# Kernel optimization log

Hardware: AMD Instinct MI355X
Metric: run time of the kernel (lower is better)

## Reference

```python
import jax, jax.numpy as jnp
import numpy as np

B, N, K = 8, 1024, 1024
C1, C2 = 64, 128
EPS = 1e-5
XTOL = 1e-7


def _skew(w):
    x, y, z = w[..., 0], w[..., 1], w[..., 2]
    o = jnp.zeros_like(x)
    r0 = jnp.stack([o, -z, y], axis=-1)
    r1 = jnp.stack([z, o, -x], axis=-1)
    r2 = jnp.stack([-y, x, o], axis=-1)
    return jnp.stack([r0, r1, r2], axis=-2)


def _expmap(dx):
    # se(3) exponential map, twist = [w(3), v(3)] -> [B,4,4]
    w, v = dx[:, :3], dx[:, 3:]
    t = jnp.linalg.norm(w, axis=1)
    W = _skew(w)
    S = jnp.matmul(W, W)
    t2 = t * t
    small = t < 1e-4
    ts = jnp.where(small, jnp.ones_like(t), t)
    s1 = jnp.where(small, 1.0 - t2 / 6.0, jnp.sin(ts) / ts)            # sin(t)/t
    s2 = jnp.where(small, 0.5 - t2 / 24.0, (1.0 - jnp.cos(ts)) / (ts * ts))  # (1-cos t)/t^2
    s3 = jnp.where(small, 1.0 / 6.0 - t2 / 120.0, (ts - jnp.sin(ts)) / (ts * ts * ts))  # (t-sin t)/t^3
    I = jnp.eye(3, dtype=dx.dtype)
    R = I + s1[:, None, None] * W + s2[:, None, None] * S
    V = I + s2[:, None, None] * W + s3[:, None, None] * S
    p = jnp.einsum('bij,bj->bi', V, v)
    g = jnp.zeros((dx.shape[0], 4, 4), dtype=dx.dtype)
    g = g.at[:, :3, :3].set(R).at[:, :3, 3].set(p).at[:, 3, 3].set(1.0)
    return g


def _transform(g, p):
    # g: [B,4,4] rigid transforms, p: [B,N,3]
    return jnp.einsum('bij,bnj->bni', g[:, :3, :3], p) + g[:, None, :3, 3]


def _bn_eval(x, gamma, beta, rm, rv_):
    # eval-mode batchnorm over channel dim of [B,C,N]
    return gamma[:, None] * (x - rm[:, None]) * jax.lax.rsqrt(rv_[:, None] + EPS) + beta[:, None]


def _pointnet(p, params, with_jac=False):
    # shared-MLP PointNet: conv1x1 -> BN(eval) -> ReLU (x3), then max-pool over points
    x = jnp.swapaxes(p, 1, 2)  # [B,3,N]
    masks = []
    for (Wt, b, gamma, beta, rm, rv_) in params:
        x = jnp.einsum('oc,bcn->bon', Wt, x) + b[:, None]
        x = _bn_eval(x, gamma, beta, rm, rv_)
        x = jnp.maximum(x, 0.0)
        if with_jac:
            masks.append((x > 0.0).astype(x.dtype))
    f = jnp.max(x, axis=-1)  # [B,K]
    if with_jac:
        return f, masks, jnp.argmax(x, axis=-1)  # max_idx [B,K]
    return f


def _cal_pinv(p0, params, masks, max_idx):
    # analytical Jacobian (Cal_Jac) + Gauss-Newton pseudo-inverse
    bsz, npts = p0.shape[0], p0.shape[1]
    W1, W2, W3 = params[0][0], params[1][0], params[2][0]
    d1 = params[0][2] * jax.lax.rsqrt(params[0][5] + EPS)  # dBN/dx in eval mode (per channel)
    d2 = params[1][2] * jax.lax.rsqrt(params[1][5] + EPS)
    d3 = params[2][2] * jax.lax.rsqrt(params[2][5] + EPS)
    D1 = d1[None, :, None] * masks[0]  # [B,C1,N]
    D2 = d2[None, :, None] * masks[1]  # [B,C2,N]
    D3 = d3[None, :, None] * masks[2]  # [B,K,N]
    # feature jacobian chain d f / d p : [B,K,N,3]
    t1 = jnp.einsum('ci,bcn->bnic', W1, D1)            # [B,N,3,C1]
    t2 = jnp.einsum('bnic,dc,bdn->bnid', t1, W2, D2)   # [B,N,3,C2]
    fj = jnp.einsum('bnid,kd,bkn->bkni', t2, W3, D3)   # [B,K,N,3]
    # warp jacobian at identity twist: [-[p]x | -I3] -> [B,N,3,6]
    eye3 = jnp.broadcast_to(jnp.eye(3, dtype=p0.dtype), (bsz, npts, 3, 3))
    warp = jnp.concatenate([-_skew(p0), -eye3], axis=-1)
    # gather the argmax point per feature channel (only rows surviving max-pool)
    fjg = jnp.take_along_axis(fj, max_idx[:, :, None, None], axis=2)[:, :, 0, :]  # [B,K,3]
    wg = jnp.take_along_axis(warp.reshape(bsz, npts, 18), max_idx[:, :, None], axis=1)
    wg = wg.reshape(bsz, -1, 3, 6)  # [B,K,3,6]
    J = jnp.einsum('bki,bkim->bkm', fjg, wg)  # [B,K,6]
    H = jnp.einsum('bki,bkj->bij', J, J)      # [B,6,6]
    pinv = jnp.einsum('bij,bkj->bik', jnp.linalg.inv(H), J)  # [B,6,K]
    return pinv


def _forward(p0, p1, W1, b1, gamma1, beta1, rm1, rv1, W2, b2, gamma2, beta2, rm2, rv2, W3, b3, gamma3, beta3, rm3, rv3, maxiter):
    params = [(W1, b1, gamma1, beta1, rm1, rv1),
              (W2, b2, gamma2, beta2, rm2, rv2),
              (W3, b3, gamma3, beta3, rm3, rv3)]
    f0, masks, max_idx = _pointnet(p0, params, with_jac=True)
    pinv = _cal_pinv(p0, params, masks, max_idx)
    bsz = p0.shape[0]
    g0 = jnp.broadcast_to(jnp.eye(4, dtype=p0.dtype), (bsz, 4, 4))

    def step(carry, _):
        g, r, done = carry
        p = _transform(g, p1)
        f = _pointnet(p, params)
        r_new = jnp.where(done, r, f - f0)           # freeze residual after xtol break
        dx = jnp.einsum('bik,bk->bi', pinv, r_new)   # Gauss-Newton step [B,6]
        conv = jnp.max(jnp.linalg.norm(dx, axis=1)) < XTOL
        stop = done | conv
        g_new = jnp.where(stop, g, jnp.matmul(_expmap(dx), g))
        return (g_new, r_new, stop), None

    init = (g0, jnp.zeros_like(f0), jnp.array(False))
    (g, r, _), _ = jax.lax.scan(step, init, None, length=maxiter)
    return r


def setup_inputs():
    key = jax.random.key(0)
    ks = jax.random.split(key, 24)
    f32 = jnp.float32
    rn = lambda i, s, sc=1.0: jax.random.normal(ks[i], s, dtype=f32) * sc
    ru = lambda i, s: jax.random.uniform(ks[i], s, dtype=f32, minval=0.5, maxval=1.5)
    p0 = rn(0, (B, N, 3))
    inp = {
        'p0': p0,
        'p1': p0 + rn(1, (B, N, 3), 0.02),  # small rigid-ish perturbation -> meaningful registration
        'W1': rn(2, (C1, 3), 0.5), 'b1': rn(3, (C1,), 0.1),
        'gamma1': ru(4, (C1,)), 'beta1': rn(5, (C1,), 0.1),
        'rm1': rn(6, (C1,), 0.1), 'rv1': ru(7, (C1,)),
        'W2': rn(8, (C2, C1), 0.2), 'b2': rn(9, (C2,), 0.1),
        'gamma2': ru(10, (C2,)), 'beta2': rn(11, (C2,), 0.1),
        'rm2': rn(12, (C2,), 0.1), 'rv2': ru(13, (C2,)),
        'W3': rn(14, (K, C2), 0.1), 'b3': rn(15, (K,), 0.1),
        'gamma3': ru(16, (K,)), 'beta3': rn(17, (K,), 0.1),
        'rm3': rn(18, (K,), 0.1), 'rv3': ru(19, (K,)),
        'maxiter': 10,
    }
    return inp


def reference(p0, p1, W1, b1, gamma1, beta1, rm1, rv1, W2, b2, gamma2, beta2, rm2, rv2, W3, b3, gamma3, beta3, rm3, rv3, maxiter):
    return _forward(p0, p1, W1, b1, gamma1, beta1, rm1, rv1, W2, b2, gamma2, beta2, rm2, rv2, W3, b3, gamma3, beta3, rm3, rv3, maxiter)
```

## Files before the change

kernel.cpp:

```cpp
#include <hip/hip_runtime.h>

#define B_ 8
#define N_ 1024
#define C1_ 64
#define C2_ 128
#define K_ 1024
#define EPS_ 1e-5f
#define XTOL_ 1e-7f

#define OFF_G      0
#define OFF_F0     128
#define OFF_PM     8320
#define OFF_M1     24704
#define OFF_M2     41088
#define OFF_SC3    73856
#define OFF_OFF3   74880
#define OFF_OFF2   75904
#define OFF_W1F    76032
#define OFF_W3HI   76288
#define OFF_W3LO   141824
#define OFF_W2H    207360
#define OFF_W2L    211456
#define OFF_J      215552
#define OFF_PINVT  264704
#define OFF_PART   330240
#define OFF_DXG    461312
#define OFF_NRM    461360
#define OFF_CNT    461368

typedef __attribute__((ext_vector_type(8))) short bf16x8;
typedef __attribute__((ext_vector_type(4))) float f32x4;

static __device__ inline unsigned short f2bf(float x) {
    unsigned u = __float_as_uint(x);
    unsigned r = (u + 0x7FFFu + ((u >> 16) & 1u)) >> 16;
    return (unsigned short)r;
}
static __device__ inline float bf2f(unsigned short h) {
    return __uint_as_float(((unsigned)h) << 16);
}
static __device__ inline unsigned pk2(unsigned short a, unsigned short b) {
    return (unsigned)a | ((unsigned)b << 16);
}

__global__ __launch_bounds__(256)
void k_prep(const float* __restrict__ W3, const float* __restrict__ b3,
            const float* __restrict__ ga3, const float* __restrict__ be3,
            const float* __restrict__ rm3, const float* __restrict__ rv3,
            const float* __restrict__ W1, const float* __restrict__ b1,
            const float* __restrict__ ga1, const float* __restrict__ be1,
            const float* __restrict__ rm1, const float* __restrict__ rv1,
            const float* __restrict__ W2, const float* __restrict__ b2,
            const float* __restrict__ ga2, const float* __restrict__ be2,
            const float* __restrict__ rm2, const float* __restrict__ rv2,
            unsigned short* __restrict__ w3hi, unsigned short* __restrict__ w3lo,
            float* __restrict__ sc3, float* __restrict__ off3,
            unsigned short* __restrict__ w2h, unsigned short* __restrict__ w2l,
            float* __restrict__ off2, float* __restrict__ w1f,
            unsigned int* __restrict__ cnt) {
    int gid = blockIdx.x * 256 + threadIdx.x;
    if (gid < K_ * C2_) {
        float w = W3[gid];
        unsigned short h = f2bf(w);
        w3hi[gid] = h;
        w3lo[gid] = f2bf(w - bf2f(h));
    }
    if (gid < K_) {
        float sc = ga3[gid] * rsqrtf(rv3[gid] + EPS_);
        sc3[gid] = sc;
        off3[gid] = sc * (b3[gid] - rm3[gid]) + be3[gid];
    }
    if (gid < C2_ * C1_) {
        int o = gid >> 6, c = gid & 63;
        float sc = ga2[o] * rsqrtf(rv2[o] + EPS_);
        float v = W2[o * C1_ + c] * sc;
        unsigned short h = f2bf(v);
        w2h[o * C1_ + c] = h;
        w2l[o * C1_ + c] = f2bf(v - bf2f(h));
    }
    if (gid < C2_) {
        float sc = ga2[gid] * rsqrtf(rv2[gid] + EPS_);
        off2[gid] = sc * (b2[gid] - rm2[gid]) + be2[gid];
    }
    if (gid < C1_) {
        float sc = ga1[gid] * rsqrtf(rv1[gid] + EPS_);
        w1f[gid * 4 + 0] = W1[gid * 3 + 0] * sc;
        w1f[gid * 4 + 1] = W1[gid * 3 + 1] * sc;
        w1f[gid * 4 + 2] = W1[gid * 3 + 2] * sc;
        w1f[gid * 4 + 3] = sc * (b1[gid] - rm1[gid]) + be1[gid];
    }
    if (gid == 0) *cnt = 0u;
}

template<int MODE>
__global__ __launch_bounds__(1024, 4)
void k_fused(const float* __restrict__ pts, const float* __restrict__ g,
             const float* __restrict__ w1f,
             const unsigned short* __restrict__ w2h, const unsigned short* __restrict__ w2l,
             const float* __restrict__ off2,
             const unsigned short* __restrict__ w3hi, const unsigned short* __restrict__ w3lo,
             const float* __restrict__ sc3, const float* __restrict__ off3,
             unsigned long long* __restrict__ part,
             unsigned long long* __restrict__ m1b, unsigned int* __restrict__ m2q) {
    __shared__ __align__(16) unsigned short a1h[128][72];
    __shared__ __align__(16) unsigned short a1l[128][72];
    __shared__ __align__(16) unsigned short sB[2][128][136];
    __shared__ float sSc[256], sOff[256], sOff2[C2_];
    __shared__ unsigned int m1w[2][128];
    __shared__ unsigned int m2w[4][128];
    __shared__ unsigned long long pmL[256];

    int slab = blockIdx.x;
    int b    = blockIdx.y;
    int q    = blockIdx.z;
    int n0   = slab * 128;
    int tx   = threadIdx.x;
    int w    = tx >> 6;
    int l    = tx & 63;
    int l15  = l & 15;
    int lhi  = l >> 4;

    if (tx < 256) { sSc[tx] = sc3[q * 256 + tx]; sOff[tx] = off3[q * 256 + tx]; }
    if (tx < C2_) sOff2[tx] = off2[tx];
    if (MODE == 0 && tx < 128) {
        m1w[0][tx] = 0u; m1w[1][tx] = 0u;
        m2w[0][tx] = 0u; m2w[1][tx] = 0u; m2w[2][tx] = 0u; m2w[3][tx] = 0u;
    }
    __syncthreads();

    {
        int n = tx & 127;
        int cgi = tx >> 7;
        const float* pp = pts + (b * N_ + n0 + n) * 3;
        float px = pp[0], py = pp[1], pz = pp[2];
        float q0, q1, q2;
        if (MODE == 1) {
            const float* gb = g + b * 16;
            q0 = fmaf(gb[0], px, fmaf(gb[1], py, fmaf(gb[2],  pz, gb[3])));
            q1 = fmaf(gb[4], px, fmaf(gb[5], py, fmaf(gb[6],  pz, gb[7])));
            q2 = fmaf(gb[8], px, fmaf(gb[9], py, fmaf(gb[10], pz, gb[11])));
        } else {
            q0 = px; q1 = py; q2 = pz;
        }
        unsigned int bits = 0u;
        unsigned hw[4], lw[4];
        #pragma unroll
        for (int j = 0; j < 8; ++j) {
            int c = cgi * 8 + j;
            float4 wf = *(const float4*)(w1f + c * 4);
            float y = fmaxf(fmaf(wf.x, q0, fmaf(wf.y, q1, fmaf(wf.z, q2, wf.w))), 0.f);
            unsigned short h = f2bf(y);
            unsigned short lo = f2bf(y - bf2f(h));
            if (j & 1) { hw[j >> 1] |= ((unsigned)h) << 16; lw[j >> 1] |= ((unsigned)lo) << 16; }
            else       { hw[j >> 1] = (unsigned)h;          lw[j >> 1] = (unsigned)lo; }
            if (MODE == 0) bits |= ((unsigned int)(y > 0.f)) << j;
        }
        uint4 vh; vh.x = hw[0]; vh.y = hw[1]; vh.z = hw[2]; vh.w = hw[3];
        uint4 vl; vl.x = lw[0]; vl.y = lw[1]; vl.z = lw[2]; vl.w = lw[3];
        *(uint4*)&a1h[n][cgi * 8] = vh;
        *(uint4*)&a1l[n][cgi * 8] = vl;
        if (MODE == 0) atomicOr(&m1w[cgi >> 2][n], bits << ((cgi & 3) * 8));
    }
    __syncthreads();

    {
        int og = w & 7;
        int nh = (w >> 3) * 4;
        f32x4 acc2[4];
        #pragma unroll
        for (int nfi = 0; nfi < 4; ++nfi) acc2[nfi] = (f32x4){0.f, 0.f, 0.f, 0.f};
        #pragma unroll
        for (int ks = 0; ks < 2; ++ks) {
            int k0 = ks * 32;
            int aoff = (og * 16 + l15) * C1_ + k0 + lhi * 8;
            bf16x8 ah2 = *(const bf16x8*)(w2h + aoff);
            bf16x8 al2 = *(const bf16x8*)(w2l + aoff);
            #pragma unroll
            for (int nfi = 0; nfi < 4; ++nfi) {
                int n = (nh + nfi) * 16 + l15;
                bf16x8 bh2 = *(const bf16x8*)&a1h[n][k0 + lhi * 8];
                bf16x8 bl2 = *(const bf16x8*)&a1l[n][k0 + lhi * 8];
                acc2[nfi] = __builtin_amdgcn_mfma_f32_16x16x32_bf16(ah2, bh2, acc2[nfi], 0, 0, 0);
                acc2[nfi] = __builtin_amdgcn_mfma_f32_16x16x32_bf16(ah2, bl2, acc2[nfi], 0, 0, 0);
                acc2[nfi] = __builtin_amdgcn_mfma_f32_16x16x32_bf16(al2, bh2, acc2[nfi], 0, 0, 0);
            }
        }
        #pragma unroll
        for (int nfi = 0; nfi < 4; ++nfi) {
            int n = (nh + nfi) * 16 + l15;
            unsigned short h4[4], l4[4];
            #pragma unroll
            for (int r = 0; r < 4; ++r) {
                int o = og * 16 + lhi * 4 + r;
                float y = fmaxf(acc2[nfi][r] + sOff2[o], 0.f);
                unsigned short h = f2bf(y);
                h4[r] = h;
                l4[r] = f2bf(y - bf2f(h));
                if (MODE == 0 && y > 0.f) atomicOr(&m2w[o >> 5][n], 1u << (o & 31));
            }
            uint2 vh; vh.x = pk2(h4[0], h4[1]); vh.y = pk2(h4[2], h4[3]);
            uint2 vl; vl.x = pk2(l4[0], l4[1]); vl.y = pk2(l4[2], l4[3]);
            *(uint2*)&sB[0][n][og * 16 + lhi * 4] = vh;
            *(uint2*)&sB[1][n][og * 16 + lhi * 4] = vl;
        }
    }
    __syncthreads();

    if (MODE == 0 && q == 0 && tx < 128) {
        m1b[b * N_ + n0 + tx] =
            (unsigned long long)m1w[0][tx] | ((unsigned long long)m1w[1][tx] << 32);
        uint4 mv; mv.x = m2w[0][tx]; mv.y = m2w[1][tx]; mv.z = m2w[2][tx]; mv.w = m2w[3][tx];
        *(uint4*)&m2q[(b * N_ + n0 + tx) * 4] = mv;
    }

    f32x4 acc[8];
    #pragma unroll
    for (int nf = 0; nf < 8; ++nf) acc[nf] = (f32x4){0.f, 0.f, 0.f, 0.f};

    #pragma unroll
    for (int ks = 0; ks < 4; ++ks) {
        int k0 = ks * 32;
        int orow = q * 256 + w * 16 + l15;
        int off = orow * C2_ + k0 + lhi * 8;
        bf16x8 ah = *(const bf16x8*)(w3hi + off);
        bf16x8 al = *(const bf16x8*)(w3lo + off);
        #pragma unroll
        for (int nh = 0; nh < 2; ++nh) {
            bf16x8 bh[4], bl[4];
            #pragma unroll
            for (int nfi = 0; nfi < 4; ++nfi) {
                int n = (nh * 4 + nfi) * 16 + l15;
                bh[nfi] = *(const bf16x8*)&sB[0][n][k0 + lhi * 8];
                bl[nfi] = *(const bf16x8*)&sB[1][n][k0 + lhi * 8];
            }
            #pragma unroll
            for (int nfi = 0; nfi < 4; ++nfi) {
                int nf = nh * 4 + nfi;
                acc[nf] = __builtin_amdgcn_mfma_f32_16x16x32_bf16(ah, bh[nfi], acc[nf], 0, 0, 0);
                acc[nf] = __builtin_amdgcn_mfma_f32_16x16x32_bf16(ah, bl[nfi], acc[nf], 0, 0, 0);
                acc[nf] = __builtin_amdgcn_mfma_f32_16x16x32_bf16(al, bh[nfi], acc[nf], 0, 0, 0);
            }
        }
    }

    #pragma unroll
    for (int r = 0; r < 4; ++r) {
        int o_l = w * 16 + lhi * 4 + r;
        float sc = sSc[o_l], of = sOff[o_l];
        float bv = -3.4e38f;
        int bi = 0;
        #pragma unroll
        for (int nf = 0; nf < 8; ++nf) {
            float y = fmaxf(sc * acc[nf][r] + of, 0.f);
            int nn = n0 + nf * 16 + l15;
            if (y > bv) { bv = y; bi = nn; }
        }
        #pragma unroll
        for (int m = 1; m <= 8; m <<= 1) {
            float ov = __shfl_xor(bv, m);
            int oi = __shfl_xor(bi, m);
            if (ov > bv || (ov == bv && oi < bi)) { bv = ov; bi = oi; }
        }
        if (l15 == 0) {
            pmL[o_l] = ((unsigned long long)__float_as_uint(bv) << 32)
                     | (unsigned int)(~(unsigned int)bi);
        }
    }
    __syncthreads();
    if (tx < 256)
        part[(size_t)slab * (B_ * K_) + b * K_ + q * 256 + tx] = pmL[tx];
}

__global__ __launch_bounds__(256)
void k_reduce(const unsigned long long* __restrict__ part,
              unsigned long long* __restrict__ pm) {
    int gid = blockIdx.x * 256 + threadIdx.x;
    unsigned long long m = part[gid];
    #pragma unroll
    for (int s = 1; s < 8; ++s) {
        unsigned long long v = part[(size_t)s * (B_ * K_) + gid];
        m = (v > m) ? v : m;
    }
    pm[gid] = m;
}

__global__ __launch_bounds__(256)
void k_rdx(const unsigned long long* __restrict__ part,
           const float* __restrict__ f0, const float* __restrict__ pinvT,
           float* __restrict__ out, float* __restrict__ g,
           float* __restrict__ dxg, float* __restrict__ nrmg,
           unsigned int* __restrict__ cnt) {
    __shared__ float redB[4][6];
    __shared__ int isLast;
    int bb = blockIdx.x;
    int tx = threadIdx.x;
    int w = tx >> 6;
    int l = tx & 63;

    float acc[6] = {0.f, 0.f, 0.f, 0.f, 0.f, 0.f};
    #pragma unroll
    for (int half = 0; half < 4; ++half) {
        int o = half * 256 + tx;
        unsigned long long m = part[(size_t)bb * K_ + o];
        #pragma unroll
        for (int s = 1; s < 8; ++s) {
            unsigned long long v = part[(size_t)s * (B_ * K_) + bb * K_ + o];
            m = (v > m) ? v : m;
        }
        float fv = __uint_as_float((unsigned int)(m >> 32));
        float rv = fv - f0[bb * K_ + o];
        out[bb * K_ + o] = rv;
        const float4* pp = (const float4*)(pinvT + (size_t)(bb * K_ + o) * 8);
        float4 pa = pp[0], pb = pp[1];
        acc[0] += pa.x * rv; acc[1] += pa.y * rv; acc[2] += pa.z * rv;
        acc[3] += pa.w * rv; acc[4] += pb.x * rv; acc[5] += pb.y * rv;
    }
    #pragma unroll
    for (int i = 0; i < 6; ++i)
        for (int off = 32; off > 0; off >>= 1) acc[i] += __shfl_down(acc[i], off);
    if (l == 0) {
        #pragma unroll
        for (int i = 0; i < 6; ++i) redB[w][i] = acc[i];
    }
    __syncthreads();
    if (tx == 0) {
        float dx6[6];
        #pragma unroll
        for (int i = 0; i < 6; ++i) {
            dx6[i] = redB[0][i] + redB[1][i] + redB[2][i] + redB[3][i];
            atomicExch(&dxg[bb * 6 + i], dx6[i]);
        }
        atomicExch(&nrmg[bb],
                   sqrtf(dx6[0]*dx6[0] + dx6[1]*dx6[1] + dx6[2]*dx6[2]
                       + dx6[3]*dx6[3] + dx6[4]*dx6[4] + dx6[5]*dx6[5]));
    }
    __threadfence();
    __syncthreads();
    if (tx == 0) {
        unsigned int old = atomicAdd(cnt, 1u);
        isLast = (old == B_ - 1) ? 1 : 0;
        if (isLast) atomicExch(cnt, 0u);
    }
    __syncthreads();
    if (!isLast) return;

    if (tx < B_) {
        int b = tx;
        float mx = 0.f;
        #pragma unroll
        for (int i = 0; i < B_; ++i) mx = fmaxf(mx, atomicAdd(&nrmg[i], 0.f));
        if (mx < XTOL_) return;
        float d[6];
        #pragma unroll
        for (int i = 0; i < 6; ++i) d[i] = atomicAdd(&dxg[b * 6 + i], 0.f);
        float wx = d[0], wy = d[1], wz = d[2];
        float vx = d[3], vy = d[4], vz = d[5];
        float t2 = wx*wx + wy*wy + wz*wz;
        float t = sqrtf(t2);
        float s1, s2, s3;
        if (t < 1e-4f) {
            s1 = 1.f - t2 / 6.f;
            s2 = 0.5f - t2 / 24.f;
            s3 = 1.f / 6.f - t2 / 120.f;
        } else {
            float st = sinf(t), ct = cosf(t);
            s1 = st / t;
            s2 = (1.f - ct) / t2;
            s3 = (t - st) / (t2 * t);
        }
        float W[3][3] = {{0.f, -wz, wy}, {wz, 0.f, -wx}, {-wy, wx, 0.f}};
        float S[3][3];
        #pragma unroll
        for (int i = 0; i < 3; ++i)
            #pragma unroll
            for (int j = 0; j < 3; ++j)
                S[i][j] = W[i][0]*W[0][j] + W[i][1]*W[1][j] + W[i][2]*W[2][j];
        float R[3][3], V[3][3];
        #pragma unroll
        for (int i = 0; i < 3; ++i)
            #pragma unroll
            for (int j = 0; j < 3; ++j) {
                float id = (i == j) ? 1.f : 0.f;
                R[i][j] = id + s1 * W[i][j] + s2 * S[i][j];
                V[i][j] = id + s2 * W[i][j] + s3 * S[i][j];
            }
        float p[3];
        #pragma unroll
        for (int i = 0; i < 3; ++i) p[i] = V[i][0]*vx + V[i][1]*vy + V[i][2]*vz;
        float* gb = g + b * 16;
        float go[16];
        #pragma unroll
        for (int i = 0; i < 16; ++i) go[i] = gb[i];
        #pragma unroll
        for (int i = 0; i < 3; ++i)
            #pragma unroll
            for (int j = 0; j < 4; ++j)
                gb[i * 4 + j] = R[i][0]*go[0*4+j] + R[i][1]*go[1*4+j]
                              + R[i][2]*go[2*4+j] + p[i]*go[3*4+j];
    }
}

__global__ __launch_bounds__(256)
void k_jac(const float* __restrict__ p0,
           const unsigned long long* __restrict__ m1b,
           const unsigned int* __restrict__ m2q,
           const float* __restrict__ W1, const float* __restrict__ ga1, const float* __restrict__ rv1,
           const float* __restrict__ W2, const float* __restrict__ ga2, const float* __restrict__ rv2,
           const float* __restrict__ W3, const float* __restrict__ ga3, const float* __restrict__ rv3,
           const unsigned long long* __restrict__ pm,
           float* __restrict__ f0, float* __restrict__ J) {
    __shared__ float wvs[4][128];
    int tx = threadIdx.x;
    int wv = tx >> 6;
    int l = tx & 63;
    int w = blockIdx.x * 4 + wv;
    int b = w >> 10;
    int k = w & 1023;

    unsigned long long pk = pm[b * K_ + k];
    float f0v = __uint_as_float((unsigned int)(pk >> 32));
    int ns = (int)(~(unsigned int)pk);
    if (l == 0) f0[b * K_ + k] = f0v;

    unsigned long long m1 = m1b[b * N_ + ns];
    const unsigned int* mq = m2q + (b * N_ + ns) * 4;
    unsigned int qa = mq[0], qb = mq[1], qc = mq[2], qd = mq[3];
    unsigned int blo = (l < 32) ? (qa >> l) : (qb >> (l - 32));
    unsigned int bhi = (l < 32) ? (qc >> l) : (qd >> (l - 32));

    const float* w3r = W3 + k * C2_;
    float s2a = ga2[l] * rsqrtf(rv2[l] + EPS_);
    float s2b = ga2[64 + l] * rsqrtf(rv2[64 + l] + EPS_);
    float wa = (blo & 1u) ? w3r[l] * s2a : 0.f;
    float wb = (bhi & 1u) ? w3r[64 + l] * s2b : 0.f;
    wvs[wv][l] = wa;
    wvs[wv][64 + l] = wb;
    __syncthreads();

    float v = 0.f;
    #pragma unroll 8
    for (int d = 0; d < C2_; ++d) v += wvs[wv][d] * W2[d * C1_ + l];

    float d1l = ((m1 >> l) & 1ull) ? ga1[l] * rsqrtf(rv1[l] + EPS_) : 0.f;
    float vc = v * d1l;
    float fj0 = vc * W1[l * 3 + 0];
    float fj1 = vc * W1[l * 3 + 1];
    float fj2 = vc * W1[l * 3 + 2];
    #pragma unroll
    for (int off = 32; off; off >>= 1) {
        fj0 += __shfl_xor(fj0, off);
        fj1 += __shfl_xor(fj1, off);
        fj2 += __shfl_xor(fj2, off);
    }
    if (l == 0) {
        float D3 = (f0v > 0.f) ? ga3[k] * rsqrtf(rv3[k] + EPS_) : 0.f;
        fj0 *= D3; fj1 *= D3; fj2 *= D3;
        float x = p0[(b * N_ + ns) * 3 + 0];
        float y = p0[(b * N_ + ns) * 3 + 1];
        float z = p0[(b * N_ + ns) * 3 + 2];
        float* Jr = J + (b * K_ + k) * 6;
        Jr[0] = fj1 * (-z) + fj2 * y;
        Jr[1] = fj0 * z    + fj2 * (-x);
        Jr[2] = fj0 * (-y) + fj1 * x;
        Jr[3] = -fj0;
        Jr[4] = -fj1;
        Jr[5] = -fj2;
    }
}

__global__ void k_hpinv(const float* __restrict__ J, float* __restrict__ pinvT,
                        float* __restrict__ g) {
    int b = blockIdx.x;
    int tx = threadIdx.x;
    __shared__ float red[256][22];
    __shared__ float hinv[36];

    if (tx < 16) g[b * 16 + tx] = (tx % 5 == 0) ? 1.f : 0.f;

    float h[21];
    #pragma unroll
    for (int q = 0; q < 21; ++q) h[q] = 0.f;
    for (int k = tx; k < K_; k += 256) {
        const float* Jr = J + (b * K_ + k) * 6;
        float jv[6] = {Jr[0], Jr[1], Jr[2], Jr[3], Jr[4], Jr[5]};
        int q = 0;
        #pragma unroll
        for (int i = 0; i < 6; ++i)
            #pragma unroll
            for (int jj = i; jj < 6; ++jj) h[q++] += jv[i] * jv[jj];
    }
    #pragma unroll
    for (int q = 0; q < 21; ++q) red[tx][q] = h[q];
    __syncthreads();
    for (int s = 128; s > 0; s >>= 1) {
        if (tx < s)
            for (int q = 0; q < 21; ++q) red[tx][q] += red[tx + s][q];
        __syncthreads();
    }
    if (tx == 0) {
        float A[6][6], Inv[6][6];
        {
            int q = 0;
            #pragma unroll
            for (int i = 0; i < 6; ++i)
                #pragma unroll
                for (int jj = i; jj < 6; ++jj) { A[i][jj] = red[0][q]; A[jj][i] = red[0][q]; ++q; }
        }
        #pragma unroll
        for (int i = 0; i < 6; ++i)
            #pragma unroll
            for (int jj = 0; jj < 6; ++jj) Inv[i][jj] = (i == jj) ? 1.f : 0.f;
        #pragma unroll
        for (int col = 0; col < 6; ++col) {
            float ipv = 1.f / A[col][col];
            #pragma unroll
            for (int jj = 0; jj < 6; ++jj) { A[col][jj] *= ipv; Inv[col][jj] *= ipv; }
            #pragma unroll
            for (int r2 = 0; r2 < 6; ++r2) {
                if (r2 == col) continue;
                float f = A[r2][col];
                #pragma unroll
                for (int jj = 0; jj < 6; ++jj) {
                    A[r2][jj]   -= f * A[col][jj];
                    Inv[r2][jj] -= f * Inv[col][jj];
                }
            }
        }
        #pragma unroll
        for (int i = 0; i < 6; ++i)
            #pragma unroll
            for (int jj = 0; jj < 6; ++jj) hinv[i * 6 + jj] = Inv[i][jj];
    }
    __syncthreads();
    for (int k = tx; k < K_; k += 256) {
        const float* Jr = J + (b * K_ + k) * 6;
        float j0 = Jr[0], j1 = Jr[1], j2 = Jr[2], j3 = Jr[3], j4 = Jr[4], j5 = Jr[5];
        float* pr = pinvT + (b * K_ + k) * 8;
        #pragma unroll
        for (int i = 0; i < 6; ++i) {
            pr[i] = hinv[i * 6 + 0] * j0 + hinv[i * 6 + 1] * j1 + hinv[i * 6 + 2] * j2
                  + hinv[i * 6 + 3] * j3 + hinv[i * 6 + 4] * j4 + hinv[i * 6 + 5] * j5;
        }
        pr[6] = 0.f; pr[7] = 0.f;
    }
}

extern "C" void kernel_launch(void* const* d_in, const int* in_sizes, int n_in,
                              void* d_out, int out_size, void* d_ws, size_t ws_size,
                              hipStream_t stream) {
    const float* p0  = (const float*)d_in[0];
    const float* p1  = (const float*)d_in[1];
    const float* W1  = (const float*)d_in[2];
    const float* b1  = (const float*)d_in[3];
    const float* ga1 = (const float*)d_in[4];
    const float* be1 = (const float*)d_in[5];
    const float* rm1 = (const float*)d_in[6];
    const float* rv1 = (const float*)d_in[7];
    const float* W2  = (const float*)d_in[8];
    const float* b2  = (const float*)d_in[9];
    const float* ga2 = (const float*)d_in[10];
    const float* be2 = (const float*)d_in[11];
    const float* rm2 = (const float*)d_in[12];
    const float* rv2 = (const float*)d_in[13];
    const float* W3  = (const float*)d_in[14];
    const float* b3  = (const float*)d_in[15];
    const float* ga3 = (const float*)d_in[16];
    const float* be3 = (const float*)d_in[17];
    const float* rm3 = (const float*)d_in[18];
    const float* rv3 = (const float*)d_in[19];

    float* ws   = (float*)d_ws;
    float* g    = ws + OFF_G;
    float* f0   = ws + OFF_F0;
    unsigned long long* pm  = (unsigned long long*)(ws + OFF_PM);
    unsigned long long* m1b = (unsigned long long*)(ws + OFF_M1);
    unsigned int*       m2q = (unsigned int*)(ws + OFF_M2);
    float* sc3  = ws + OFF_SC3;
    float* off3 = ws + OFF_OFF3;
    float* off2 = ws + OFF_OFF2;
    float* w1f  = ws + OFF_W1F;
    unsigned short* w3hi = (unsigned short*)(ws + OFF_W3HI);
    unsigned short* w3lo = (unsigned short*)(ws + OFF_W3LO);
    unsigned short* w2h  = (unsigned short*)(ws + OFF_W2H);
    unsigned short* w2l  = (unsigned short*)(ws + OFF_W2L);
    float* Jb    = ws + OFF_J;
    float* pinvT = ws + OFF_PINVT;
    unsigned long long* part = (unsigned long long*)(ws + OFF_PART);
    float* dxg   = ws + OFF_DXG;
    float* nrmg  = ws + OFF_NRM;
    unsigned int* cnt = (unsigned int*)(ws + OFF_CNT);
    float* out   = (float*)d_out;

    dim3 gridF(8, B_, 4);

    k_prep<<<(K_ * C2_ + 255) / 256, 256, 0, stream>>>(
        W3, b3, ga3, be3, rm3, rv3,
        W1, b1, ga1, be1, rm1, rv1,
        W2, b2, ga2, be2, rm2, rv2,
        w3hi, w3lo, sc3, off3, w2h, w2l, off2, w1f, cnt);

    k_fused<0><<<gridF, 1024, 0, stream>>>(p0, g, w1f, w2h, w2l, off2, w3hi, w3lo,
                                           sc3, off3, part, m1b, m2q);
    k_reduce<<<B_ * K_ / 256, 256, 0, stream>>>(part, pm);
    k_jac<<<B_ * K_ / 4, 256, 0, stream>>>(p0, m1b, m2q, W1, ga1, rv1, W2, ga2, rv2,
                                           W3, ga3, rv3, pm, f0, Jb);
    k_hpinv<<<B_, 256, 0, stream>>>(Jb, pinvT, g);

    for (int it = 0; it < 10; ++it) {
        k_fused<1><<<gridF, 1024, 0, stream>>>(p1, g, w1f, w2h, w2l, off2, w3hi, w3lo,
                                               sc3, off3, part, m1b, m2q);
        k_rdx<<<B_, 256, 0, stream>>>(part, f0, pinvT, out, g, dxg, nrmg, cnt);
    }
}
```

Baseline: 257.7 us.

## Split fused MLP into two point halves to cut LDS and registers

The fused layer-2/layer-3 stage now handles the 128-point slab in two halves of 64 points. This halves the shared sB buffer and replaces the 8-wide accumulator array with a single running accumulator plus running max/argmax. The launch bound rises from 4 to 8 waves per EU, which pushes the compiler toward fewer registers per thread. The cost is reloading W2/W3 fragments per half and per tile, plus extra barriers and less ILP inside each wave.

```diff
diff --git a/kernel.cpp b/kernel.cpp
--- a/kernel.cpp
+++ b/kernel.cpp
@@ -93,7 +93,7 @@
 }
 
 template<int MODE>
-__global__ __launch_bounds__(1024, 4)
+__global__ __launch_bounds__(1024, 8)
 void k_fused(const float* __restrict__ pts, const float* __restrict__ g,
              const float* __restrict__ w1f,
              const unsigned short* __restrict__ w2h, const unsigned short* __restrict__ w2l,
@@ -104,7 +104,7 @@
              unsigned long long* __restrict__ m1b, unsigned int* __restrict__ m2q) {
     __shared__ __align__(16) unsigned short a1h[128][72];
     __shared__ __align__(16) unsigned short a1l[128][72];
-    __shared__ __align__(16) unsigned short sB[2][128][136];
+    __shared__ __align__(16) unsigned short sB[2][64][136];
     __shared__ float sSc[256], sOff[256], sOff2[C2_];
     __shared__ unsigned int m1w[2][128];
     __shared__ unsigned int m2w[4][128];
@@ -163,107 +163,110 @@
     }
     __syncthreads();
 
-    {
-        int og = w & 7;
-        int nh = (w >> 3) * 4;
-        f32x4 acc2[4];
-        #pragma unroll
-        for (int nfi = 0; nfi < 4; ++nfi) acc2[nfi] = (f32x4){0.f, 0.f, 0.f, 0.f};
-        #pragma unroll
-        for (int ks = 0; ks < 2; ++ks) {
-            int k0 = ks * 32;
-            int aoff = (og * 16 + l15) * C1_ + k0 + lhi * 8;
-            bf16x8 ah2 = *(const bf16x8*)(w2h + aoff);
-            bf16x8 al2 = *(const bf16x8*)(w2l + aoff);
-            #pragma unroll
-            for (int nfi = 0; nfi < 4; ++nfi) {
-                int n = (nh + nfi) * 16 + l15;
-                bf16x8 bh2 = *(const bf16x8*)&a1h[n][k0 + lhi * 8];
-                bf16x8 bl2 = *(const bf16x8*)&a1l[n][k0 + lhi * 8];
-                acc2[nfi] = __builtin_amdgcn_mfma_f32_16x16x32_bf16(ah2, bh2, acc2[nfi], 0, 0, 0);
-                acc2[nfi] = __builtin_amdgcn_mfma_f32_16x16x32_bf16(ah2, bl2, acc2[nfi], 0, 0, 0);
-                acc2[nfi] = __builtin_amdgcn_mfma_f32_16x16x32_bf16(al2, bh2, acc2[nfi], 0, 0, 0);
-            }
-        }
-        #pragma unroll
-        for (int nfi = 0; nfi < 4; ++nfi) {
-            int n = (nh + nfi) * 16 + l15;
-            unsigned short h4[4], l4[4];
-            #pragma unroll
-            for (int r = 0; r < 4; ++r) {
-                int o = og * 16 + lhi * 4 + r;
-                float y = fmaxf(acc2[nfi][r] + sOff2[o], 0.f);
-                unsigned short h = f2bf(y);
-                h4[r] = h;
-                l4[r] = f2bf(y - bf2f(h));
-                if (MODE == 0 && y > 0.f) atomicOr(&m2w[o >> 5][n], 1u << (o & 31));
-            }
-            uint2 vh; vh.x = pk2(h4[0], h4[1]); vh.y = pk2(h4[2], h4[3]);
-            uint2 vl; vl.x = pk2(l4[0], l4[1]); vl.y = pk2(l4[2], l4[3]);
-            *(uint2*)&sB[0][n][og * 16 + lhi * 4] = vh;
-            *(uint2*)&sB[1][n][og * 16 + lhi * 4] = vl;
-        }
-    }
-    __syncthreads();
-
     if (MODE == 0 && q == 0 && tx < 128) {
         m1b[b * N_ + n0 + tx] =
             (unsigned long long)m1w[0][tx] | ((unsigned long long)m1w[1][tx] << 32);
+    }
+
+    float bv0 = -3.4e38f, bv1 = -3.4e38f, bv2 = -3.4e38f, bv3 = -3.4e38f;
+    int   bi0 = 0, bi1 = 0, bi2 = 0, bi3 = 0;
+    float scr[4], ofr[4];
+    #pragma unroll
+    for (int r = 0; r < 4; ++r) {
+        scr[r] = sSc[w * 16 + lhi * 4 + r];
+        ofr[r] = sOff[w * 16 + lhi * 4 + r];
+    }
+
+    for (int half = 0; half < 2; ++half) {
+        {
+            int og = w & 7;
+            #pragma unroll
+            for (int ti = 0; ti < 2; ++ti) {
+                int nf_l = (w >> 3) * 2 + ti;
+                int n_l = nf_l * 16 + l15;
+                int n_g = half * 64 + n_l;
+                f32x4 acc2 = (f32x4){0.f, 0.f, 0.f, 0.f};
+                #pragma unroll
+                for (int ks = 0; ks < 2; ++ks) {
+                    int k0 = ks * 32;
+                    int aoff = (og * 16 + l15) * C1_ + k0 + lhi * 8;
+                    bf16x8 ah2 = *(const bf16x8*)(w2h + aoff);
+                    bf16x8 al2 = *(const bf16x8*)(w2l + aoff);
+                    bf16x8 bh2 = *(const bf16x8*)&a1h[n_g][k0 + lhi * 8];
+                    bf16x8 bl2 = *(const bf16x8*)&a1l[n_g][k0 + lhi * 8];
+                    acc2 = __builtin_amdgcn_mfma_f32_16x16x32_bf16(ah2, bh2, acc2, 0, 0, 0);
+                    acc2 = __builtin_amdgcn_mfma_f32_16x16x32_bf16(ah2, bl2, acc2, 0, 0, 0);
+                    acc2 = __builtin_amdgcn_mfma_f32_16x16x32_bf16(al2, bh2, acc2, 0, 0, 0);
+                }
+                unsigned short h4[4], l4[4];
+                #pragma unroll
+                for (int r = 0; r < 4; ++r) {
+                    int o = og * 16 + lhi * 4 + r;
+                    float y = fmaxf(acc2[r] + sOff2[o], 0.f);
+                    unsigned short h = f2bf(y);
+                    h4[r] = h;
+                    l4[r] = f2bf(y - bf2f(h));
+                    if (MODE == 0 && y > 0.f) atomicOr(&m2w[o >> 5][n_g], 1u << (o & 31));
+                }
+                uint2 vh; vh.x = pk2(h4[0], h4[1]); vh.y = pk2(h4[2], h4[3]);
+                uint2 vl; vl.x = pk2(l4[0], l4[1]); vl.y = pk2(l4[2], l4[3]);
+                *(uint2*)&sB[0][n_l][og * 16 + lhi * 4] = vh;
+                *(uint2*)&sB[1][n_l][og * 16 + lhi * 4] = vl;
+            }
+        }
+        __syncthreads();
+
+        #pragma unroll
+        for (int nf_l = 0; nf_l < 4; ++nf_l) {
+            int n_l = nf_l * 16 + l15;
+            f32x4 acc = (f32x4){0.f, 0.f, 0.f, 0.f};
+            #pragma unroll
+            for (int ks = 0; ks < 4; ++ks) {
+                int k0 = ks * 32;
+                int orow = q * 256 + w * 16 + l15;
+                int off = orow * C2_ + k0 + lhi * 8;
+                bf16x8 ah = *(const bf16x8*)(w3hi + off);
+                bf16x8 al = *(const bf16x8*)(w3lo + off);
+                bf16x8 bh = *(const bf16x8*)&sB[0][n_l][k0 + lhi * 8];
+                bf16x8 bl = *(const bf16x8*)&sB[1][n_l][k0 + lhi * 8];
+                acc = __builtin_amdgcn_mfma_f32_16x16x32_bf16(ah, bh, acc, 0, 0, 0);
+                acc = __builtin_amdgcn_mfma_f32_16x16x32_bf16(ah, bl, acc, 0, 0, 0);
+                acc = __builtin_amdgcn_mfma_f32_16x16x32_bf16(al, bh, acc, 0, 0, 0);
+            }
+            int nn = n0 + half * 64 + nf_l * 16 + l15;
+            float y0 = fmaxf(scr[0] * acc[0] + ofr[0], 0.f);
+            float y1 = fmaxf(scr[1] * acc[1] + ofr[1], 0.f);
+            float y2 = fmaxf(scr[2] * acc[2] + ofr[2], 0.f);
+            float y3 = fmaxf(scr[3] * acc[3] + ofr[3], 0.f);
+            if (y0 > bv0) { bv0 = y0; bi0 = nn; }
+            if (y1 > bv1) { bv1 = y1; bi1 = nn; }
+            if (y2 > bv2) { bv2 = y2; bi2 = nn; }
+            if (y3 > bv3) { bv3 = y3; bi3 = nn; }
+        }
+        __syncthreads();
+    }
+
+    if (MODE == 0 && q == 0 && tx < 128) {
         uint4 mv; mv.x = m2w[0][tx]; mv.y = m2w[1][tx]; mv.z = m2w[2][tx]; mv.w = m2w[3][tx];
         *(uint4*)&m2q[(b * N_ + n0 + tx) * 4] = mv;
     }
 
-    f32x4 acc[8];
-    #pragma unroll
-    for (int nf = 0; nf < 8; ++nf) acc[nf] = (f32x4){0.f, 0.f, 0.f, 0.f};
-
-    #pragma unroll
-    for (int ks = 0; ks < 4; ++ks) {
-        int k0 = ks * 32;
-        int orow = q * 256 + w * 16 + l15;
-        int off = orow * C2_ + k0 + lhi * 8;
-        bf16x8 ah = *(const bf16x8*)(w3hi + off);
-        bf16x8 al = *(const bf16x8*)(w3lo + off);
-        #pragma unroll
-        for (int nh = 0; nh < 2; ++nh) {
-            bf16x8 bh[4], bl[4];
-            #pragma unroll
-            for (int nfi = 0; nfi < 4; ++nfi) {
-                int n = (nh * 4 + nfi) * 16 + l15;
-                bh[nfi] = *(const bf16x8*)&sB[0][n][k0 + lhi * 8];
-                bl[nfi] = *(const bf16x8*)&sB[1][n][k0 + lhi * 8];
+    {
+        float bv[4] = {bv0, bv1, bv2, bv3};
+        int   bi[4] = {bi0, bi1, bi2, bi3};
+        #pragma unroll
+        for (int r = 0; r < 4; ++r) {
+            #pragma unroll
+            for (int m = 1; m <= 8; m <<= 1) {
+                float ov = __shfl_xor(bv[r], m);
+                int oi = __shfl_xor(bi[r], m);
+                if (ov > bv[r] || (ov == bv[r] && oi < bi[r])) { bv[r] = ov; bi[r] = oi; }
             }
-            #pragma unroll
-            for (int nfi = 0; nfi < 4; ++nfi) {
-                int nf = nh * 4 + nfi;
-                acc[nf] = __builtin_amdgcn_mfma_f32_16x16x32_bf16(ah, bh[nfi], acc[nf], 0, 0, 0);
-                acc[nf] = __builtin_amdgcn_mfma_f32_16x16x32_bf16(ah, bl[nfi], acc[nf], 0, 0, 0);
-                acc[nf] = __builtin_amdgcn_mfma_f32_16x16x32_bf16(al, bh[nfi], acc[nf], 0, 0, 0);
+            if (l15 == 0) {
+                pmL[w * 16 + lhi * 4 + r] =
+                    ((unsigned long long)__float_as_uint(bv[r]) << 32)
+                    | (unsigned int)(~(unsigned int)bi[r]);
             }
-        }
-    }
-
-    #pragma unroll
-    for (int r = 0; r < 4; ++r) {
-        int o_l = w * 16 + lhi * 4 + r;
-        float sc = sSc[o_l], of = sOff[o_l];
-        float bv = -3.4e38f;
-        int bi = 0;
-        #pragma unroll
-        for (int nf = 0; nf < 8; ++nf) {
-            float y = fmaxf(sc * acc[nf][r] + of, 0.f);
-            int nn = n0 + nf * 16 + l15;
-            if (y > bv) { bv = y; bi = nn; }
-        }
-        #pragma unroll
-        for (int m = 1; m <= 8; m <<= 1) {
-            float ov = __shfl_xor(bv, m);
-            int oi = __shfl_xor(bi, m);
-            if (ov > bv || (ov == bv && oi < bi)) { bv = ov; bi = oi; }
-        }
-        if (l15 == 0) {
-            pmL[o_l] = ((unsigned long long)__float_as_uint(bv) << 32)
-                     | (unsigned int)(~(unsigned int)bi);
         }
     }
     __syncthreads();
```

Result: slower. 407.9 us (+58.3%).

## Retile fused PointNet kernel to 256-point slabs and 128-channel output groups

Applied to the files above, without the earlier changes.

Changes the fused kernel's work split from 8 point-slabs × 4 output quarters to 4 point-slabs of 256 × 8 output groups of 128. Each block now processes its slab in two halves, recomputing layer 2 per half and keeping running argmax in registers. This halves the number of partial-max slabs the reduce kernels must combine and gives more reuse of each slab's layer-1 activations. In exchange, layer 2 is recomputed across 8 output groups instead of 4, which doubles the redundant conv2 work, and the larger layer-1 shared buffers raise LDS use.

```diff
diff --git a/kernel.cpp b/kernel.cpp
--- a/kernel.cpp
+++ b/kernel.cpp
@@ -102,35 +102,36 @@
              const float* __restrict__ sc3, const float* __restrict__ off3,
              unsigned long long* __restrict__ part,
              unsigned long long* __restrict__ m1b, unsigned int* __restrict__ m2q) {
-    __shared__ __align__(16) unsigned short a1h[128][72];
-    __shared__ __align__(16) unsigned short a1l[128][72];
+    __shared__ __align__(16) unsigned short a1h[256][72];
+    __shared__ __align__(16) unsigned short a1l[256][72];
     __shared__ __align__(16) unsigned short sB[2][128][136];
-    __shared__ float sSc[256], sOff[256], sOff2[C2_];
-    __shared__ unsigned int m1w[2][128];
-    __shared__ unsigned int m2w[4][128];
-    __shared__ unsigned long long pmL[256];
+    __shared__ float sSc[128], sOff[128], sOff2[C2_];
+    __shared__ unsigned int m1w[2][256];
+    __shared__ unsigned int m2w[4][256];
+    __shared__ unsigned long long pmW[2][128];
 
     int slab = blockIdx.x;
     int b    = blockIdx.y;
-    int q    = blockIdx.z;
-    int n0   = slab * 128;
+    int oq   = blockIdx.z;
+    int n0   = slab * 256;
+    int ob   = oq * 128;
     int tx   = threadIdx.x;
     int w    = tx >> 6;
     int l    = tx & 63;
     int l15  = l & 15;
     int lhi  = l >> 4;
 
-    if (tx < 256) { sSc[tx] = sc3[q * 256 + tx]; sOff[tx] = off3[q * 256 + tx]; }
+    if (tx < 128) { sSc[tx] = sc3[ob + tx]; sOff[tx] = off3[ob + tx]; }
     if (tx < C2_) sOff2[tx] = off2[tx];
-    if (MODE == 0 && tx < 128) {
+    if (MODE == 0 && tx < 256) {
         m1w[0][tx] = 0u; m1w[1][tx] = 0u;
         m2w[0][tx] = 0u; m2w[1][tx] = 0u; m2w[2][tx] = 0u; m2w[3][tx] = 0u;
     }
     __syncthreads();
 
     {
-        int n = tx & 127;
-        int cgi = tx >> 7;
+        int n = tx & 255;
+        int cgi = tx >> 8;
         const float* pp = pts + (b * N_ + n0 + n) * 3;
         float px = pp[0], py = pp[1], pz = pp[2];
         float q0, q1, q2;
@@ -143,10 +144,10 @@
             q0 = px; q1 = py; q2 = pz;
         }
         unsigned int bits = 0u;
-        unsigned hw[4], lw[4];
-        #pragma unroll
-        for (int j = 0; j < 8; ++j) {
-            int c = cgi * 8 + j;
+        unsigned hw[8], lw[8];
+        #pragma unroll
+        for (int j = 0; j < 16; ++j) {
+            int c = cgi * 16 + j;
             float4 wf = *(const float4*)(w1f + c * 4);
             float y = fmaxf(fmaf(wf.x, q0, fmaf(wf.y, q1, fmaf(wf.z, q2, wf.w))), 0.f);
             unsigned short h = f2bf(y);
@@ -155,106 +156,120 @@
             else       { hw[j >> 1] = (unsigned)h;          lw[j >> 1] = (unsigned)lo; }
             if (MODE == 0) bits |= ((unsigned int)(y > 0.f)) << j;
         }
-        uint4 vh; vh.x = hw[0]; vh.y = hw[1]; vh.z = hw[2]; vh.w = hw[3];
-        uint4 vl; vl.x = lw[0]; vl.y = lw[1]; vl.z = lw[2]; vl.w = lw[3];
-        *(uint4*)&a1h[n][cgi * 8] = vh;
-        *(uint4*)&a1l[n][cgi * 8] = vl;
-        if (MODE == 0) atomicOr(&m1w[cgi >> 2][n], bits << ((cgi & 3) * 8));
-    }
-    __syncthreads();
-
-    {
-        int og = w & 7;
-        int nh = (w >> 3) * 4;
-        f32x4 acc2[4];
-        #pragma unroll
-        for (int nfi = 0; nfi < 4; ++nfi) acc2[nfi] = (f32x4){0.f, 0.f, 0.f, 0.f};
-        #pragma unroll
-        for (int ks = 0; ks < 2; ++ks) {
-            int k0 = ks * 32;
-            int aoff = (og * 16 + l15) * C1_ + k0 + lhi * 8;
-            bf16x8 ah2 = *(const bf16x8*)(w2h + aoff);
-            bf16x8 al2 = *(const bf16x8*)(w2l + aoff);
+        uint4 v0; v0.x = hw[0]; v0.y = hw[1]; v0.z = hw[2]; v0.w = hw[3];
+        uint4 v1; v1.x = hw[4]; v1.y = hw[5]; v1.z = hw[6]; v1.w = hw[7];
+        *(uint4*)&a1h[n][cgi * 16 + 0] = v0;
+        *(uint4*)&a1h[n][cgi * 16 + 8] = v1;
+        uint4 v2; v2.x = lw[0]; v2.y = lw[1]; v2.z = lw[2]; v2.w = lw[3];
+        uint4 v3; v3.x = lw[4]; v3.y = lw[5]; v3.z = lw[6]; v3.w = lw[7];
+        *(uint4*)&a1l[n][cgi * 16 + 0] = v2;
+        *(uint4*)&a1l[n][cgi * 16 + 8] = v3;
+        if (MODE == 0) atomicOr(&m1w[cgi >> 1][n], bits << ((cgi & 1) * 16));
+    }
+    __syncthreads();
+
+    int og3 = w & 7;
+    int nfh = w >> 3;
+    float bvr[4];
+    int   bir[4];
+    float scr[4], ofr[4];
+    #pragma unroll
+    for (int r = 0; r < 4; ++r) {
+        bvr[r] = -3.4e38f; bir[r] = 0;
+        scr[r] = sSc[og3 * 16 + lhi * 4 + r];
+        ofr[r] = sOff[og3 * 16 + lhi * 4 + r];
+    }
+
+    for (int half = 0; half < 2; ++half) {
+        {
+            int og = w & 7;
+            int nh = (w >> 3) * 4;
+            f32x4 acc2[4];
+            #pragma unroll
+            for (int nfi = 0; nfi < 4; ++nfi) acc2[nfi] = (f32x4){0.f, 0.f, 0.f, 0.f};
+            #pragma unroll
+            for (int ks = 0; ks < 2; ++ks) {
+                int k0 = ks * 32;
+                int aoff = (og * 16 + l15) * C1_ + k0 + lhi * 8;
+                bf16x8 ah2 = *(const bf16x8*)(w2h + aoff);
+                bf16x8 al2 = *(const bf16x8*)(w2l + aoff);
+                #pragma unroll
+                for (int nfi = 0; nfi < 4; ++nfi) {
+                    int n_g = half * 128 + (nh + nfi) * 16 + l15;
+                    bf16x8 bh2 = *(const bf16x8*)&a1h[n_g][k0 + lhi * 8];
+                    bf16x8 bl2 = *(const bf16x8*)&a1l[n_g][k0 + lhi * 8];
+                    acc2[nfi] = __builtin_amdgcn_mfma_f32_16x16x32_bf16(ah2, bh2, acc2[nfi], 0, 0, 0);
+                    acc2[nfi] = __builtin_amdgcn_mfma_f32_16x16x32_bf16(ah2, bl2, acc2[nfi], 0, 0, 0);
+                    acc2[nfi] = __builtin_amdgcn_mfma_f32_16x16x32_bf16(al2, bh2, acc2[nfi], 0, 0, 0);
+                }
+            }
             #pragma unroll
             for (int nfi = 0; nfi < 4; ++nfi) {
-                int n = (nh + nfi) * 16 + l15;
-                bf16x8 bh2 = *(const bf16x8*)&a1h[n][k0 + lhi * 8];
-                bf16x8 bl2 = *(const bf16x8*)&a1l[n][k0 + lhi * 8];
-                acc2[nfi] = __builtin_amdgcn_mfma_f32_16x16x32_bf16(ah2, bh2, acc2[nfi], 0, 0, 0);
-                acc2[nfi] = __builtin_amdgcn_mfma_f32_16x16x32_bf16(ah2, bl2, acc2[nfi], 0, 0, 0);
-                acc2[nfi] = __builtin_amdgcn_mfma_f32_16x16x32_bf16(al2, bh2, acc2[nfi], 0, 0, 0);
+                int n_l = (nh + nfi) * 16 + l15;
+                int n_g = half * 128 + n_l;
+                unsigned short h4[4], l4[4];
+                #pragma unroll
+                for (int r = 0; r < 4; ++r) {
+                    int o = og * 16 + lhi * 4 + r;
+                    float y = fmaxf(acc2[nfi][r] + sOff2[o], 0.f);
+                    unsigned short h = f2bf(y);
+                    h4[r] = h;
+                    l4[r] = f2bf(y - bf2f(h));
+                    if (MODE == 0 && y > 0.f) atomicOr(&m2w[o >> 5][n_g], 1u << (o & 31));
+                }
+                uint2 vh; vh.x = pk2(h4[0], h4[1]); vh.y = pk2(h4[2], h4[3]);
+                uint2 vl; vl.x = pk2(l4[0], l4[1]); vl.y = pk2(l4[2], l4[3]);
+                *(uint2*)&sB[0][n_l][og * 16 + lhi * 4] = vh;
+                *(uint2*)&sB[1][n_l][og * 16 + lhi * 4] = vl;
             }
         }
-        #pragma unroll
-        for (int nfi = 0; nfi < 4; ++nfi) {
-            int n = (nh + nfi) * 16 + l15;
-            unsigned short h4[4], l4[4];
-            #pragma unroll
-            for (int r = 0; r < 4; ++r) {
-                int o = og * 16 + lhi * 4 + r;
-                float y = fmaxf(acc2[nfi][r] + sOff2[o], 0.f);
-                unsigned short h = f2bf(y);
-                h4[r] = h;
-                l4[r] = f2bf(y - bf2f(h));
-                if (MODE == 0 && y > 0.f) atomicOr(&m2w[o >> 5][n], 1u << (o & 31));
+        __syncthreads();
+
+        {
+            f32x4 acc3[4];
+            #pragma unroll
+            for (int nfi = 0; nfi < 4; ++nfi) acc3[nfi] = (f32x4){0.f, 0.f, 0.f, 0.f};
+            #pragma unroll
+            for (int ks = 0; ks < 4; ++ks) {
+                int k0 = ks * 32;
+                int orow = ob + og3 * 16 + l15;
+                int off = orow * C2_ + k0 + lhi * 8;
+                bf16x8 ah = *(const bf16x8*)(w3hi + off);
+                bf16x8 al = *(const bf16x8*)(w3lo + off);
+                #pragma unroll
+                for (int nfi = 0; nfi < 4; ++nfi) {
+                    int n_l = (nfh * 4 + nfi) * 16 + l15;
+                    bf16x8 bh = *(const bf16x8*)&sB[0][n_l][k0 + lhi * 8];
+                    bf16x8 bl = *(const bf16x8*)&sB[1][n_l][k0 + lhi * 8];
+                    acc3[nfi] = __builtin_amdgcn_mfma_f32_16x16x32_bf16(ah, bh, acc3[nfi], 0, 0, 0);
+                    acc3[nfi] = __builtin_amdgcn_mfma_f32_16x16x32_bf16(ah, bl, acc3[nfi], 0, 0, 0);
+                    acc3[nfi] = __builtin_amdgcn_mfma_f32_16x16x32_bf16(al, bh, acc3[nfi], 0, 0, 0);
+                }
             }
-            uint2 vh; vh.x = pk2(h4[0], h4[1]); vh.y = pk2(h4[2], h4[3]);
-            uint2 vl; vl.x = pk2(l4[0], l4[1]); vl.y = pk2(l4[2], l4[3]);
-            *(uint2*)&sB[0][n][og * 16 + lhi * 4] = vh;
-            *(uint2*)&sB[1][n][og * 16 + lhi * 4] = vl;
-        }
-    }
-    __syncthreads();
-
-    if (MODE == 0 && q == 0 && tx < 128) {
+            #pragma unroll
+            for (int nfi = 0; nfi < 4; ++nfi) {
+                int nn = n0 + half * 128 + (nfh * 4 + nfi) * 16 + l15;
+                #pragma unroll
+                for (int r = 0; r < 4; ++r) {
+                    float y = fmaxf(scr[r] * acc3[nfi][r] + ofr[r], 0.f);
+                    if (y > bvr[r]) { bvr[r] = y; bir[r] = nn; }
+                }
+            }
+        }
+        __syncthreads();
+    }
+
+    if (MODE == 0 && oq == 0 && tx < 256) {
         m1b[b * N_ + n0 + tx] =
             (unsigned long long)m1w[0][tx] | ((unsigned long long)m1w[1][tx] << 32);
         uint4 mv; mv.x = m2w[0][tx]; mv.y = m2w[1][tx]; mv.z = m2w[2][tx]; mv.w = m2w[3][tx];
         *(uint4*)&m2q[(b * N_ + n0 + tx) * 4] = mv;
     }
 
-    f32x4 acc[8];
-    #pragma unroll
-    for (int nf = 0; nf < 8; ++nf) acc[nf] = (f32x4){0.f, 0.f, 0.f, 0.f};
-
-    #pragma unroll
-    for (int ks = 0; ks < 4; ++ks) {
-        int k0 = ks * 32;
-        int orow = q * 256 + w * 16 + l15;
-        int off = orow * C2_ + k0 + lhi * 8;
-        bf16x8 ah = *(const bf16x8*)(w3hi + off);
-        bf16x8 al = *(const bf16x8*)(w3lo + off);
-        #pragma unroll
-        for (int nh = 0; nh < 2; ++nh) {
-            bf16x8 bh[4], bl[4];
-            #pragma unroll
-            for (int nfi = 0; nfi < 4; ++nfi) {
-                int n = (nh * 4 + nfi) * 16 + l15;
-                bh[nfi] = *(const bf16x8*)&sB[0][n][k0 + lhi * 8];
-                bl[nfi] = *(const bf16x8*)&sB[1][n][k0 + lhi * 8];
-            }
-            #pragma unroll
-            for (int nfi = 0; nfi < 4; ++nfi) {
-                int nf = nh * 4 + nfi;
-                acc[nf] = __builtin_amdgcn_mfma_f32_16x16x32_bf16(ah, bh[nfi], acc[nf], 0, 0, 0);
-                acc[nf] = __builtin_amdgcn_mfma_f32_16x16x32_bf16(ah, bl[nfi], acc[nf], 0, 0, 0);
-                acc[nf] = __builtin_amdgcn_mfma_f32_16x16x32_bf16(al, bh[nfi], acc[nf], 0, 0, 0);
-            }
-        }
-    }
-
     #pragma unroll
     for (int r = 0; r < 4; ++r) {
-        int o_l = w * 16 + lhi * 4 + r;
-        float sc = sSc[o_l], of = sOff[o_l];
-        float bv = -3.4e38f;
-        int bi = 0;
-        #pragma unroll
-        for (int nf = 0; nf < 8; ++nf) {
-            float y = fmaxf(sc * acc[nf][r] + of, 0.f);
-            int nn = n0 + nf * 16 + l15;
-            if (y > bv) { bv = y; bi = nn; }
-        }
+        float bv = bvr[r];
+        int bi = bir[r];
         #pragma unroll
         for (int m = 1; m <= 8; m <<= 1) {
             float ov = __shfl_xor(bv, m);
@@ -262,13 +277,17 @@
             if (ov > bv || (ov == bv && oi < bi)) { bv = ov; bi = oi; }
         }
         if (l15 == 0) {
-            pmL[o_l] = ((unsigned long long)__float_as_uint(bv) << 32)
-                     | (unsigned int)(~(unsigned int)bi);
-        }
-    }
-    __syncthreads();
-    if (tx < 256)
-        part[(size_t)slab * (B_ * K_) + b * K_ + q * 256 + tx] = pmL[tx];
+            pmW[nfh][og3 * 16 + lhi * 4 + r] =
+                ((unsigned long long)__float_as_uint(bv) << 32)
+                | (unsigned int)(~(unsigned int)bi);
+        }
+    }
+    __syncthreads();
+    if (tx < 128) {
+        unsigned long long a = pmW[0][tx], c = pmW[1][tx];
+        unsigned long long m = (c > a) ? c : a;
+        part[(size_t)slab * (B_ * K_) + b * K_ + ob + tx] = m;
+    }
 }
 
 __global__ __launch_bounds__(256)
@@ -277,7 +296,7 @@
     int gid = blockIdx.x * 256 + threadIdx.x;
     unsigned long long m = part[gid];
     #pragma unroll
-    for (int s = 1; s < 8; ++s) {
+    for (int s = 1; s < 4; ++s) {
         unsigned long long v = part[(size_t)s * (B_ * K_) + gid];
         m = (v > m) ? v : m;
     }
@@ -303,7 +322,7 @@
         int o = half * 256 + tx;
         unsigned long long m = part[(size_t)bb * K_ + o];
         #pragma unroll
-        for (int s = 1; s < 8; ++s) {
+        for (int s = 1; s < 4; ++s) {
             unsigned long long v = part[(size_t)s * (B_ * K_) + bb * K_ + o];
             m = (v > m) ? v : m;
         }
@@ -591,7 +610,7 @@
     unsigned int* cnt = (unsigned int*)(ws + OFF_CNT);
     float* out   = (float*)d_out;
 
-    dim3 gridF(8, B_, 4);
+    dim3 gridF(4, B_, 8);
 
     k_prep<<<(K_ * C2_ + 255) / 256, 256, 0, stream>>>(
         W3, b3, ga3, be3, rm3, rv3,
```

Result: slower. 313.0 us (+21.4%).
